# Performance work log

Hardware: AMD Instinct MI355X
Metric: run time of the kernel (lower is better)

Reference implementation:

```python
import jax, jax.numpy as jnp
import numpy as np

N_NODES = 200000
DIM_NODE = 128
DIM_NIG = 128
DIM_HIDDEN = 256
BATCH = 8192


def setup_inputs() -> dict:
    key = jax.random.key(0)
    ks = jax.random.split(key, 16)
    s = 0.05
    inp = {
        "src_node_ids": jnp.arange(BATCH, dtype=jnp.int64),
        "dst_node_ids": jnp.arange(BATCH, dtype=jnp.int64),
        "src_previous_embedding": jax.random.normal(ks[0], (N_NODES, DIM_NODE), jnp.float32),
        "dst_previous_embedding": jax.random.normal(ks[1], (N_NODES, DIM_NODE), jnp.float32),
        "batch_src_neighbor_embedding": jax.random.normal(ks[2], (BATCH, DIM_NIG), jnp.float32),
        "batch_dst_neighbor_embedding": jax.random.normal(ks[3], (BATCH, DIM_NIG), jnp.float32),
        # Linear params stored as [in, out]; forward is x @ W + b (== torch x @ W_t.T + b)
        "W_src_nig": jax.random.normal(ks[4], (DIM_NIG, DIM_HIDDEN), jnp.float32) * s,
        "b_src_nig": jnp.zeros((DIM_HIDDEN,), jnp.float32),
        "W_src_resize": jax.random.normal(ks[5], (DIM_NODE, DIM_HIDDEN), jnp.float32) * s,
        "b_src_resize": jnp.zeros((DIM_HIDDEN,), jnp.float32),
        "W_src_out": jax.random.normal(ks[6], (2 * DIM_HIDDEN, DIM_NODE), jnp.float32) * s,
        "b_src_out": jnp.zeros((DIM_NODE,), jnp.float32),
        "W_dst_nig": jax.random.normal(ks[7], (DIM_NIG, DIM_HIDDEN), jnp.float32) * s,
        "b_dst_nig": jnp.zeros((DIM_HIDDEN,), jnp.float32),
        "W_dst_resize": jax.random.normal(ks[8], (DIM_NODE, DIM_HIDDEN), jnp.float32) * s,
        "b_dst_resize": jnp.zeros((DIM_HIDDEN,), jnp.float32),
        "W_dst_out": jax.random.normal(ks[9], (2 * DIM_HIDDEN, DIM_NODE), jnp.float32) * s,
        "b_dst_out": jnp.zeros((DIM_NODE,), jnp.float32),
    }
    return inp


def _update_side(ids, prev_emb, nig_emb, W_nig, b_nig, W_resize, b_resize, W_out, b_out):
    # gather rows [B, dim_node] -> resize to hidden
    sel = prev_emb[ids] @ W_resize + b_resize            # [B, H]
    shift = nig_emb @ W_nig + b_nig                      # [B, H]
    node_emb = jnp.concatenate([sel, shift], axis=1) @ W_out + b_out  # [B, dim_node]
    # clone().detach() then scatter-write rows
    return prev_emb.at[ids].set(node_emb)


def reference(src_node_ids, dst_node_ids, src_previous_embedding, dst_previous_embedding,
              batch_src_neighbor_embedding, batch_dst_neighbor_embedding,
              W_src_nig, b_src_nig, W_src_resize, b_src_resize, W_src_out, b_src_out,
              W_dst_nig, b_dst_nig, W_dst_resize, b_dst_resize, W_dst_out, b_dst_out):
    updated_src = _update_side(src_node_ids, src_previous_embedding, batch_src_neighbor_embedding,
                               W_src_nig, b_src_nig, W_src_resize, b_src_resize, W_src_out, b_src_out)
    updated_dst = _update_side(dst_node_ids, dst_previous_embedding, batch_dst_neighbor_embedding,
                               W_dst_nig, b_dst_nig, W_dst_resize, b_dst_resize, W_dst_out, b_dst_out)
    return (updated_src, updated_dst)
```

## Files before the change

kernel.cpp:

```cpp
#include <hip/hip_runtime.h>

#define N_NODES 200000
#define DIM 128
#define HID 256
#define BATCH 8192
#define SIDE_FLOATS (N_NODES * DIM)
#define MAGIC 0x5EED1234u

typedef float vf4 __attribute__((ext_vector_type(4)));

__global__ __launch_bounds__(128) void setup_kernel(
    const float* __restrict__ Wr0, const float* __restrict__ Wn0, const float* __restrict__ Wo0,
    const float* __restrict__ br0, const float* __restrict__ bn0, const float* __restrict__ bo0,
    const float* __restrict__ Wr1, const float* __restrict__ Wn1, const float* __restrict__ Wo1,
    const float* __restrict__ br1, const float* __restrict__ bn1, const float* __restrict__ bo1,
    const int* __restrict__ ids0, const int* __restrict__ ids1,
    float* __restrict__ Mf, float* __restrict__ bias,
    unsigned* __restrict__ flags0, unsigned* __restrict__ flags1)
{
    const int s = blockIdx.y;
    const int j = threadIdx.x;
    const int k = blockIdx.x;

    if (k < 2 * DIM) {
        const float* Wr = s ? Wr1 : Wr0;
        const float* Wn = s ? Wn1 : Wn0;
        const float* Wo = s ? Wo1 : Wo0;
        __shared__ float w[HID];
        const float* wrow = (k < DIM) ? (Wr + k * HID) : (Wn + (k - DIM) * HID);
        const float* wo   = (k < DIM) ? Wo : (Wo + HID * DIM);
        w[j]       = wrow[j];
        w[j + DIM] = wrow[j + DIM];
        __syncthreads();
        float acc = 0.f;
        #pragma unroll 8
        for (int h = 0; h < HID; ++h) acc += w[h] * wo[h * DIM + j];
        Mf[((s << 8) + k) * DIM + j] = acc;
    } else if (k == 2 * DIM) {
        const float* Wo = s ? Wo1 : Wo0;
        const float* br = s ? br1 : br0;
        const float* bn = s ? bn1 : bn0;
        const float* bo = s ? bo1 : bo0;
        float acc = bo[j];
        for (int h = 0; h < HID; ++h) acc += br[h] * Wo[h * DIM + j];
        for (int h = 0; h < HID; ++h) acc += bn[h] * Wo[(HID + h) * DIM + j];
        bias[s * DIM + j] = acc;
    } else {
        const int i = (k - (2 * DIM + 1)) * 128 + j;
        const int* ids   = s ? ids1 : ids0;
        unsigned*  fl    = s ? flags1 : flags0;
        fl[ids[i]] = MAGIC;
    }
}

#define RB 32
#define CAT_STRIDE 260

#define COPY_BLOCKS_PER_SIDE 4096
#define ROW_GROUPS 25000

__global__ __launch_bounds__(256) void fused_kernel(
    const int* __restrict__ ids0, const float* __restrict__ prev0, const float* __restrict__ nig0,
    const int* __restrict__ ids1, const float* __restrict__ prev1, const float* __restrict__ nig1,
    const float* __restrict__ Mf, const float* __restrict__ bias,
    const unsigned* __restrict__ flags0, const unsigned* __restrict__ flags1,
    float* __restrict__ out)
{
    const int bx  = blockIdx.x;
    const int tid = threadIdx.x;

    if (bx < 512) {
        const int s = bx >> 8;
        const int*   ids  = s ? ids1  : ids0;
        const float* prev = s ? prev1 : prev0;
        const float* nig  = s ? nig1  : nig0;
        const float* M    = Mf + s * (2 * DIM) * DIM;
        const float* bs   = bias + s * DIM;
        float* outs = out + (size_t)s * SIDE_FLOATS;

        __shared__ int   sid[RB];
        __shared__ float cat[RB][CAT_STRIDE];

        const int b0 = (bx & 255) * RB;

        if (tid < RB) sid[tid] = ids[b0 + tid];
        __syncthreads();

        for (int idx = tid; idx < RB * 64; idx += 256) {
            const int r = idx >> 6;
            const int q = idx & 63;
            float4 v;
            if (q < 32) v = ((const float4*)(prev + (size_t)sid[r] * DIM))[q];
            else        v = ((const float4*)(nig  + (size_t)(b0 + r) * DIM))[q - 32];
            *(float4*)&cat[r][q * 4] = v;
        }
        __syncthreads();

        const int jg = tid & 31;
        const int rg = tid >> 5;

        float acc[4][4];
        #pragma unroll
        for (int r = 0; r < 4; ++r)
            #pragma unroll
            for (int c = 0; c < 4; ++c) acc[r][c] = 0.f;

        const float4* M4 = (const float4*)M;
        #pragma unroll 4
        for (int k = 0; k < 2 * DIM; ++k) {
            const float4 m = M4[(k << 5) + jg];
            #pragma unroll
            for (int r = 0; r < 4; ++r) {
                const float a = cat[rg * 4 + r][k];
                acc[r][0] += a * m.x;
                acc[r][1] += a * m.y;
                acc[r][2] += a * m.z;
                acc[r][3] += a * m.w;
            }
        }

        const float4 bj = ((const float4*)bs)[jg];
        #pragma unroll
        for (int r = 0; r < 4; ++r) {
            const int row = sid[rg * 4 + r];
            float4 v;
            v.x = acc[r][0] + bj.x;
            v.y = acc[r][1] + bj.y;
            v.z = acc[r][2] + bj.z;
            v.w = acc[r][3] + bj.w;
            ((float4*)(outs + (size_t)row * DIM))[jg] = v;
        }
        return;
    }

    const int cb   = bx - 512;
    const int side = cb >> 12;
    const int c    = cb & (COPY_BLOCKS_PER_SIDE - 1);
    const vf4*      p4 = (const vf4*)(side ? prev1 : prev0);
    const unsigned* fl = side ? flags1 : flags0;
    vf4* o4 = (vf4*)out + (size_t)side * (SIDE_FLOATS / 4);

    const int rloc = tid >> 5;
    const int q    = tid & 31;

    #pragma unroll 2
    for (int g = c; g < ROW_GROUPS; g += COPY_BLOCKS_PER_SIDE) {
        const int row = (g << 3) + rloc;
        if (fl[row] != MAGIC) {
            const size_t idx = (size_t)row * 32 + q;
            vf4 v = __builtin_nontemporal_load(p4 + idx);
            __builtin_nontemporal_store(v, o4 + idx);
        }
    }
}

extern "C" void kernel_launch(void* const* d_in, const int* in_sizes, int n_in,
                              void* d_out, int out_size, void* d_ws, size_t ws_size,
                              hipStream_t stream) {
    const int*   src_ids   = (const int*)d_in[0];
    const int*   dst_ids   = (const int*)d_in[1];
    const float* src_prev  = (const float*)d_in[2];
    const float* dst_prev  = (const float*)d_in[3];
    const float* src_nig   = (const float*)d_in[4];
    const float* dst_nig   = (const float*)d_in[5];
    const float* W_src_nig     = (const float*)d_in[6];
    const float* b_src_nig     = (const float*)d_in[7];
    const float* W_src_resize  = (const float*)d_in[8];
    const float* b_src_resize  = (const float*)d_in[9];
    const float* W_src_out     = (const float*)d_in[10];
    const float* b_src_out     = (const float*)d_in[11];
    const float* W_dst_nig     = (const float*)d_in[12];
    const float* b_dst_nig     = (const float*)d_in[13];
    const float* W_dst_resize  = (const float*)d_in[14];
    const float* b_dst_resize  = (const float*)d_in[15];
    const float* W_dst_out     = (const float*)d_in[16];
    const float* b_dst_out     = (const float*)d_in[17];

    float* out  = (float*)d_out;
    float* Mf   = (float*)d_ws;
    float* bias = Mf + 2 * (2 * DIM) * DIM;
    unsigned* flags0 = (unsigned*)(bias + 2 * DIM);
    unsigned* flags1 = flags0 + N_NODES;

    setup_kernel<<<dim3(2 * DIM + 1 + BATCH / 128, 2), 128, 0, stream>>>(
        W_src_resize, W_src_nig, W_src_out, b_src_resize, b_src_nig, b_src_out,
        W_dst_resize, W_dst_nig, W_dst_out, b_dst_resize, b_dst_nig, b_dst_out,
        src_ids, dst_ids, Mf, bias, flags0, flags1);

    fused_kernel<<<512 + 2 * COPY_BLOCKS_PER_SIDE, 256, 0, stream>>>(
        src_ids, src_prev, src_nig,
        dst_ids, dst_prev, dst_nig,
        Mf, bias, flags0, flags1, out);
}
```

Measured before the change: 404.2 us.

## Copy full embedding tables alongside weight folding, then scatter updated rows after

```diff
diff --git a/kernel.cpp b/kernel.cpp
--- a/kernel.cpp
+++ b/kernel.cpp
@@ -5,152 +5,145 @@
 #define HID 256
 #define BATCH 8192
 #define SIDE_FLOATS (N_NODES * DIM)
-#define MAGIC 0x5EED1234u
+#define SIDE_F4 (SIDE_FLOATS / 4)
 
 typedef float vf4 __attribute__((ext_vector_type(4)));
 
-__global__ __launch_bounds__(128) void setup_kernel(
+#define SETUP_BLOCKS 514
+#define COPY_BLOCKS_PER_SIDE 4096
+#define COPY_THREADS_PER_SIDE (COPY_BLOCKS_PER_SIDE * 256)
+
+__global__ __launch_bounds__(256) void copy_setup_kernel(
+    const float* __restrict__ prev0, const float* __restrict__ prev1,
     const float* __restrict__ Wr0, const float* __restrict__ Wn0, const float* __restrict__ Wo0,
     const float* __restrict__ br0, const float* __restrict__ bn0, const float* __restrict__ bo0,
     const float* __restrict__ Wr1, const float* __restrict__ Wn1, const float* __restrict__ Wo1,
     const float* __restrict__ br1, const float* __restrict__ bn1, const float* __restrict__ bo1,
-    const int* __restrict__ ids0, const int* __restrict__ ids1,
     float* __restrict__ Mf, float* __restrict__ bias,
-    unsigned* __restrict__ flags0, unsigned* __restrict__ flags1)
+    float* __restrict__ out)
 {
-    const int s = blockIdx.y;
-    const int j = threadIdx.x;
-    const int k = blockIdx.x;
+    const int bx  = blockIdx.x;
+    const int tid = threadIdx.x;
+
+    if (bx >= SETUP_BLOCKS) {
+        const int cb   = bx - SETUP_BLOCKS;
+        const int side = cb >> 12;
+        const int c    = cb & (COPY_BLOCKS_PER_SIDE - 1);
+        const vf4* __restrict__ p4 = (const vf4*)(side ? prev1 : prev0);
+        vf4* o4 = (vf4*)out + (size_t)side * SIDE_F4;
+
+        int idx = c * 256 + tid;
+        #pragma unroll
+        for (int i = 0; i < 7; ++i) {
+            if (idx < SIDE_F4) {
+                vf4 v = __builtin_nontemporal_load(p4 + idx);
+                __builtin_nontemporal_store(v, o4 + idx);
+            }
+            idx += COPY_THREADS_PER_SIDE;
+        }
+        return;
+    }
+
+    const int s = (bx >= 257) ? 1 : 0;
+    const int k = bx - s * 257;
+    const float* Wr = s ? Wr1 : Wr0;
+    const float* Wn = s ? Wn1 : Wn0;
+    const float* Wo = s ? Wo1 : Wo0;
 
     if (k < 2 * DIM) {
-        const float* Wr = s ? Wr1 : Wr0;
-        const float* Wn = s ? Wn1 : Wn0;
-        const float* Wo = s ? Wo1 : Wo0;
         __shared__ float w[HID];
         const float* wrow = (k < DIM) ? (Wr + k * HID) : (Wn + (k - DIM) * HID);
         const float* wo   = (k < DIM) ? Wo : (Wo + HID * DIM);
-        w[j]       = wrow[j];
-        w[j + DIM] = wrow[j + DIM];
+        w[tid] = wrow[tid];
         __syncthreads();
-        float acc = 0.f;
-        #pragma unroll 8
-        for (int h = 0; h < HID; ++h) acc += w[h] * wo[h * DIM + j];
-        Mf[((s << 8) + k) * DIM + j] = acc;
-    } else if (k == 2 * DIM) {
-        const float* Wo = s ? Wo1 : Wo0;
+        if (tid < DIM) {
+            float acc = 0.f;
+            #pragma unroll 8
+            for (int h = 0; h < HID; ++h) acc += w[h] * wo[h * DIM + tid];
+            Mf[((s << 8) + k) * DIM + tid] = acc;
+        }
+    } else if (tid < DIM) {
         const float* br = s ? br1 : br0;
         const float* bn = s ? bn1 : bn0;
         const float* bo = s ? bo1 : bo0;
-        float acc = bo[j];
-        for (int h = 0; h < HID; ++h) acc += br[h] * Wo[h * DIM + j];
-        for (int h = 0; h < HID; ++h) acc += bn[h] * Wo[(HID + h) * DIM + j];
-        bias[s * DIM + j] = acc;
-    } else {
-        const int i = (k - (2 * DIM + 1)) * 128 + j;
-        const int* ids   = s ? ids1 : ids0;
-        unsigned*  fl    = s ? flags1 : flags0;
-        fl[ids[i]] = MAGIC;
+        float acc = bo[tid];
+        for (int h = 0; h < HID; ++h) acc += br[h] * Wo[h * DIM + tid];
+        for (int h = 0; h < HID; ++h) acc += bn[h] * Wo[(HID + h) * DIM + tid];
+        bias[s * DIM + tid] = acc;
     }
 }
 
 #define RB 32
 #define CAT_STRIDE 260
 
-#define COPY_BLOCKS_PER_SIDE 4096
-#define ROW_GROUPS 25000
-
-__global__ __launch_bounds__(256) void fused_kernel(
+__global__ __launch_bounds__(256) void update_kernel(
     const int* __restrict__ ids0, const float* __restrict__ prev0, const float* __restrict__ nig0,
     const int* __restrict__ ids1, const float* __restrict__ prev1, const float* __restrict__ nig1,
     const float* __restrict__ Mf, const float* __restrict__ bias,
-    const unsigned* __restrict__ flags0, const unsigned* __restrict__ flags1,
     float* __restrict__ out)
 {
     const int bx  = blockIdx.x;
     const int tid = threadIdx.x;
 
-    if (bx < 512) {
-        const int s = bx >> 8;
-        const int*   ids  = s ? ids1  : ids0;
-        const float* prev = s ? prev1 : prev0;
-        const float* nig  = s ? nig1  : nig0;
-        const float* M    = Mf + s * (2 * DIM) * DIM;
-        const float* bs   = bias + s * DIM;
-        float* outs = out + (size_t)s * SIDE_FLOATS;
+    const int s = bx >> 8;
+    const int*   ids  = s ? ids1  : ids0;
+    const float* prev = s ? prev1 : prev0;
+    const float* nig  = s ? nig1  : nig0;
+    const float* M    = Mf + s * (2 * DIM) * DIM;
+    const float* bs   = bias + s * DIM;
+    float* outs = out + (size_t)s * SIDE_FLOATS;
 
-        __shared__ int   sid[RB];
-        __shared__ float cat[RB][CAT_STRIDE];
+    __shared__ int   sid[RB];
+    __shared__ float cat[RB][CAT_STRIDE];
 
-        const int b0 = (bx & 255) * RB;
+    const int b0 = (bx & 255) * RB;
 
-        if (tid < RB) sid[tid] = ids[b0 + tid];
-        __syncthreads();
+    if (tid < RB) sid[tid] = ids[b0 + tid];
+    __syncthreads();
 
-        for (int idx = tid; idx < RB * 64; idx += 256) {
-            const int r = idx >> 6;
-            const int q = idx & 63;
-            float4 v;
-            if (q < 32) v = ((const float4*)(prev + (size_t)sid[r] * DIM))[q];
-            else        v = ((const float4*)(nig  + (size_t)(b0 + r) * DIM))[q - 32];
-            *(float4*)&cat[r][q * 4] = v;
-        }
-        __syncthreads();
+    for (int idx = tid; idx < RB * 64; idx += 256) {
+        const int r = idx >> 6;
+        const int q = idx & 63;
+        float4 v;
+        if (q < 32) v = ((const float4*)(prev + (size_t)sid[r] * DIM))[q];
+        else        v = ((const float4*)(nig  + (size_t)(b0 + r) * DIM))[q - 32];
+        *(float4*)&cat[r][q * 4] = v;
+    }
+    __syncthreads();
 
-        const int jg = tid & 31;
-        const int rg = tid >> 5;
+    const int jg = tid & 31;
+    const int rg = tid >> 5;
 
-        float acc[4][4];
+    float acc[4][4];
+    #pragma unroll
+    for (int r = 0; r < 4; ++r)
         #pragma unroll
-        for (int r = 0; r < 4; ++r)
-            #pragma unroll
-            for (int c = 0; c < 4; ++c) acc[r][c] = 0.f;
+        for (int c = 0; c < 4; ++c) acc[r][c] = 0.f;
 
-        const float4* M4 = (const float4*)M;
-        #pragma unroll 4
-        for (int k = 0; k < 2 * DIM; ++k) {
-            const float4 m = M4[(k << 5) + jg];
-            #pragma unroll
-            for (int r = 0; r < 4; ++r) {
-                const float a = cat[rg * 4 + r][k];
-                acc[r][0] += a * m.x;
-                acc[r][1] += a * m.y;
-                acc[r][2] += a * m.z;
-                acc[r][3] += a * m.w;
-            }
-        }
-
-        const float4 bj = ((const float4*)bs)[jg];
+    const float4* M4 = (const float4*)M;
+    #pragma unroll 4
+    for (int k = 0; k < 2 * DIM; ++k) {
+        const float4 m = M4[(k << 5) + jg];
         #pragma unroll
         for (int r = 0; r < 4; ++r) {
-            const int row = sid[rg * 4 + r];
-            float4 v;
-            v.x = acc[r][0] + bj.x;
-            v.y = acc[r][1] + bj.y;
-            v.z = acc[r][2] + bj.z;
-            v.w = acc[r][3] + bj.w;
-            ((float4*)(outs + (size_t)row * DIM))[jg] = v;
+            const float a = cat[rg * 4 + r][k];
+            acc[r][0] += a * m.x;
+            acc[r][1] += a * m.y;
+            acc[r][2] += a * m.z;
+            acc[r][3] += a * m.w;
         }
-        return;
     }
 
-    const int cb   = bx - 512;
-    const int side = cb >> 12;
-    const int c    = cb & (COPY_BLOCKS_PER_SIDE - 1);
-    const vf4*      p4 = (const vf4*)(side ? prev1 : prev0);
-    const unsigned* fl = side ? flags1 : flags0;
-    vf4* o4 = (vf4*)out + (size_t)side * (SIDE_FLOATS / 4);
-
-    const int rloc = tid >> 5;
-    const int q    = tid & 31;
-
-    #pragma unroll 2
-    for (int g = c; g < ROW_GROUPS; g += COPY_BLOCKS_PER_SIDE) {
-        const int row = (g << 3) + rloc;
-        if (fl[row] != MAGIC) {
-            const size_t idx = (size_t)row * 32 + q;
-            vf4 v = __builtin_nontemporal_load(p4 + idx);
-            __builtin_nontemporal_store(v, o4 + idx);
-        }
+    const float4 bj = ((const float4*)bs)[jg];
+    #pragma unroll
+    for (int r = 0; r < 4; ++r) {
+        const int row = sid[rg * 4 + r];
+        float4 v;
+        v.x = acc[r][0] + bj.x;
+        v.y = acc[r][1] + bj.y;
+        v.z = acc[r][2] + bj.z;
+        v.w = acc[r][3] + bj.w;
+        ((float4*)(outs + (size_t)row * DIM))[jg] = v;
     }
 }
 
@@ -179,16 +172,15 @@
     float* out  = (float*)d_out;
     float* Mf   = (float*)d_ws;
     float* bias = Mf + 2 * (2 * DIM) * DIM;
-    unsigned* flags0 = (unsigned*)(bias + 2 * DIM);
-    unsigned* flags1 = flags0 + N_NODES;
 
-    setup_kernel<<<dim3(2 * DIM + 1 + BATCH / 128, 2), 128, 0, stream>>>(
+    copy_setup_kernel<<<SETUP_BLOCKS + 2 * COPY_BLOCKS_PER_SIDE, 256, 0, stream>>>(
+        src_prev, dst_prev,
         W_src_resize, W_src_nig, W_src_out, b_src_resize, b_src_nig, b_src_out,
         W_dst_resize, W_dst_nig, W_dst_out, b_dst_resize, b_dst_nig, b_dst_out,
-        src_ids, dst_ids, Mf, bias, flags0, flags1);
+        Mf, bias, out);
 
-    fused_kernel<<<512 + 2 * COPY_BLOCKS_PER_SIDE, 256, 0, stream>>>(
+    update_kernel<<<512, 256, 0, stream>>>(
         src_ids, src_prev, src_nig,
         dst_ids, dst_prev, dst_nig,
-        Mf, bias, flags0, flags1, out);
+        Mf, bias, out);
 }
```

Measured after the change: 400.1 us. About the same (-1.0%).
